# Kernel tuning notes

Measured on AMD Instinct MI355X. Metric: run time of the kernel, lower is better.

Reference implementation:

```python
import jax, jax.numpy as jnp
import numpy as np

EPS = 1e-12  # torch F.normalize eps

def _l2norm(v, axis):
    n = jnp.sqrt(jnp.sum(v * v, axis=axis, keepdims=True))
    return v / jnp.maximum(n, EPS)

def setup_inputs() -> dict:
    key = jax.random.key(0)
    k1, k2, k3, k4, k5 = jax.random.split(key, 5)
    N, C, D, K, R = 8, 1024, 128, 64, 256
    return {
        "x": jax.random.normal(k1, (N, C, D), dtype=jnp.float32),
        "cluster": jax.random.normal(k2, (N, R, D), dtype=jnp.float32),
        "conv_w": jax.random.normal(k3, (K, D), dtype=jnp.float32) * 0.1,
        "conv_b": jax.random.normal(k4, (K,), dtype=jnp.float32) * 0.1,
        "cluster_idx": jax.random.randint(k5, (K,), 0, R),
    }

def reference(x, cluster, conv_w, conv_b, cluster_idx):
    # x: (N, C, D); cluster: (N, R, D); conv_w: (K, D); conv_b: (K,)
    x = _l2norm(x, -1)  # normalize_input, descriptor-wise L2 over dim
    # Conv1d(dim->K, kernel=1) on x^T == matmul over D; softmax over clusters K
    logits = jnp.einsum('ncd,kd->nkc', x, conv_w) + conv_b[None, :, None]
    soft = jax.nn.softmax(logits, axis=1)  # (N, K, C)
    cent = cluster[:, cluster_idx, :]      # (N, K, D) sampled centroids
    # broadcast residual, scaled by soft assignment (no sum over C in V2)
    residual = (x[:, None, :, :] - cent[:, :, None, :]) * soft[..., None]  # (N,K,C,D)
    vlad = jnp.swapaxes(residual, 1, 2)    # (N, C, K, D)
    vlad = _l2norm(vlad, -1)               # intra-normalize over D
    N, C, K, D = vlad.shape
    vlad = vlad.reshape(N, C, K * D)
    return _l2norm(vlad, -1)               # final L2 over flattened K*D
```

## Files before the change

### kernel.cpp

```cpp
#include <hip/hip_runtime.h>

#define N_ 8
#define C_ 1024
#define D_ 128
#define K_ 64
#define R_ 256

typedef float fvec4 __attribute__((ext_vector_type(4)));

__global__ __launch_bounds__(256) void vlad_stream_kernel(
    const float* __restrict__ x,
    const float* __restrict__ cluster,
    const int*   __restrict__ cluster_idx,
    float*       __restrict__ out)
{
    const int n   = blockIdx.x & 7;
    const int c   = blockIdx.x >> 3;
    const int blk = (n << 10) + c;
    const int t   = threadIdx.x;
    const int l   = t & 31;
    const int h   = t >> 5;

    const float* xrow = x + (size_t)blk * D_;
    fvec4 xv = *(const fvec4*)(xrow + l * 4);

    const float* cbase = cluster + (size_t)n * (R_ * D_);
    fvec4 cv[8];
    #pragma unroll
    for (int p = 0; p < 8; ++p) {
        const int k = p * 8 + h;
        cv[p] = *(const fvec4*)(cbase + (size_t)cluster_idx[k] * D_ + l * 4);
    }

    float nx = fmaf(xv.x, xv.x, fmaf(xv.y, xv.y, fmaf(xv.z, xv.z, xv.w * xv.w)));
    #pragma unroll
    for (int m = 1; m <= 16; m <<= 1) nx += __shfl_xor(nx, m, 32);
    const float rinv = 1.0f / fmaxf(sqrtf(nx), 1e-12f);
    xv *= rinv;

    float* orow = out + (size_t)blk * (K_ * D_) + (size_t)t * 4;
    #pragma unroll
    for (int p = 0; p < 8; ++p) {
        fvec4 d = xv - cv[p];
        float ds = fmaf(d.x, d.x, fmaf(d.y, d.y, fmaf(d.z, d.z, d.w * d.w)));
        #pragma unroll
        for (int m = 1; m <= 16; m <<= 1) ds += __shfl_xor(ds, m, 32);
        const float id = 0.125f / fmaxf(sqrtf(ds), 1e-12f);
        *(fvec4*)(orow + (size_t)p * 1024) = d * id;
    }
}

extern "C" void kernel_launch(void* const* d_in, const int* in_sizes, int n_in,
                              void* d_out, int out_size, void* d_ws, size_t ws_size,
                              hipStream_t stream) {
    const float* x           = (const float*)d_in[0];
    const float* cluster     = (const float*)d_in[1];
    const int*   cluster_idx = (const int*)d_in[4];
    float* out = (float*)d_out;

    dim3 grid(N_ * C_), block(256);
    vlad_stream_kernel<<<grid, block, 0, stream>>>(x, cluster, cluster_idx, out);
}
```

Measured before the change: 58.34 us.

## Tile 16 descriptor rows per block and precompute residual norms in shared memory

Each block now handles 16 rows of one batch instead of one row. It normalises the rows into shared memory and computes all 64 residual norms per row in a separate phase with a cooperative reduction. It then streams the scaled residual outputs while reusing the gathered centroid vectors across the 16 rows. The aim is to cut the block count and the redundant centroid gathers, at the cost of extra syncthreads and a serial norm phase in front of the output-write-bound store loop.

Result: no change. 59.30 us (+1.7%).

```diff
diff --git a/kernel.cpp b/kernel.cpp
--- a/kernel.cpp
+++ b/kernel.cpp
@@ -5,48 +5,88 @@
 #define D_ 128
 #define K_ 64
 #define R_ 256
+#define TC 16
+#define XPAD 132
 
 typedef float fvec4 __attribute__((ext_vector_type(4)));
 
-__global__ __launch_bounds__(256) void vlad_stream_kernel(
+__global__ __launch_bounds__(256) void vlad_tiled_kernel(
     const float* __restrict__ x,
     const float* __restrict__ cluster,
     const int*   __restrict__ cluster_idx,
     float*       __restrict__ out)
 {
-    const int n   = blockIdx.x & 7;
-    const int c   = blockIdx.x >> 3;
-    const int blk = (n << 10) + c;
+    __shared__ float xh[TC][XPAD];
+    __shared__ float id_s[TC][K_];
+    __shared__ float part1[TC][16];
+    __shared__ float rinv_s[TC];
+    __shared__ int   coff[K_];
+
+    const int bid = blockIdx.x;
+    const int n   = bid & 7;
+    const int c0  = (bid >> 3) * TC;
     const int t   = threadIdx.x;
-    const int l   = t & 31;
-    const int h   = t >> 5;
 
-    const float* xrow = x + (size_t)blk * D_;
-    fvec4 xv = *(const fvec4*)(xrow + l * 4);
+    if (t < K_) coff[t] = cluster_idx[t] * D_;
 
-    const float* cbase = cluster + (size_t)n * (R_ * D_);
+    const int r = t >> 4, s = t & 15;
+    const float* xrow = x + (size_t)(n * C_ + c0 + r) * D_ + s * 8;
+    fvec4 xa = *(const fvec4*)xrow;
+    fvec4 xb = *(const fvec4*)(xrow + 4);
+    part1[r][s] = xa.x*xa.x + xa.y*xa.y + xa.z*xa.z + xa.w*xa.w
+                + xb.x*xb.x + xb.y*xb.y + xb.z*xb.z + xb.w*xb.w;
+    __syncthreads();
+    if (t < TC) {
+        const fvec4* pp = (const fvec4*)part1[t];
+        fvec4 v = pp[0] + pp[1] + pp[2] + pp[3];
+        rinv_s[t] = 1.0f / fmaxf(sqrtf(v.x + v.y + v.z + v.w), 1e-12f);
+    }
+    __syncthreads();
+    const float rv = rinv_s[r];
+    xa *= rv; xb *= rv;
+    *(fvec4*)&xh[r][s * 8]     = xa;
+    *(fvec4*)&xh[r][s * 8 + 4] = xb;
+    __syncthreads();
+
+    {
+        const int c  = t & 15;
+        const int g  = (t >> 4) & 3;
+        const int kb = t >> 6;
+        const float* cb = cluster + (size_t)n * (R_ * D_) + g * 32;
+        fvec4 xr[8];
+        #pragma unroll
+        for (int j = 0; j < 8; ++j) xr[j] = *(const fvec4*)&xh[c][g * 32 + j * 4];
+        for (int ki = 0; ki < 16; ++ki) {
+            const int k = kb * 16 + ki;
+            const float* crow = cb + coff[k];
+            float acc = 0.f;
+            #pragma unroll
+            for (int j = 0; j < 8; ++j) {
+                fvec4 cv = *(const fvec4*)(crow + j * 4);
+                fvec4 d  = xr[j] - cv;
+                acc = fmaf(d.x, d.x, fmaf(d.y, d.y, fmaf(d.z, d.z, fmaf(d.w, d.w, acc))));
+            }
+            acc += __shfl_xor(acc, 16);
+            acc += __shfl_xor(acc, 32);
+            if (g == 0) id_s[c][k] = 0.125f / fmaxf(sqrtf(acc), 1e-12f);
+        }
+    }
+    __syncthreads();
+
+    const int d4 = t & 31, h = t >> 5;
+    const float* cb2 = cluster + (size_t)n * (R_ * D_) + d4 * 4;
     fvec4 cv[8];
     #pragma unroll
-    for (int p = 0; p < 8; ++p) {
-        const int k = p * 8 + h;
-        cv[p] = *(const fvec4*)(cbase + (size_t)cluster_idx[k] * D_ + l * 4);
-    }
-
-    float nx = fmaf(xv.x, xv.x, fmaf(xv.y, xv.y, fmaf(xv.z, xv.z, xv.w * xv.w)));
-    #pragma unroll
-    for (int m = 1; m <= 16; m <<= 1) nx += __shfl_xor(nx, m, 32);
-    const float rinv = 1.0f / fmaxf(sqrtf(nx), 1e-12f);
-    xv *= rinv;
-
-    float* orow = out + (size_t)blk * (K_ * D_) + (size_t)t * 4;
-    #pragma unroll
-    for (int p = 0; p < 8; ++p) {
-        fvec4 d = xv - cv[p];
-        float ds = fmaf(d.x, d.x, fmaf(d.y, d.y, fmaf(d.z, d.z, d.w * d.w)));
+    for (int q = 0; q < 8; ++q) cv[q] = *(const fvec4*)(cb2 + coff[q * 8 + h]);
+    float* ob = out + (size_t)(n * C_ + c0) * (K_ * D_) + h * D_ + d4 * 4;
+    for (int cc = 0; cc < TC; ++cc) {
+        const fvec4 xv = *(const fvec4*)&xh[cc][d4 * 4];
+        float* oc = ob + (size_t)cc * (K_ * D_);
         #pragma unroll
-        for (int m = 1; m <= 16; m <<= 1) ds += __shfl_xor(ds, m, 32);
-        const float id = 0.125f / fmaxf(sqrtf(ds), 1e-12f);
-        *(fvec4*)(orow + (size_t)p * 1024) = d * id;
+        for (int q = 0; q < 8; ++q) {
+            const float idv = id_s[cc][q * 8 + h];
+            *(fvec4*)(oc + q * 8 * D_) = (xv - cv[q]) * idv;
+        }
     }
 }
 
@@ -58,6 +98,6 @@
     const int*   cluster_idx = (const int*)d_in[4];
     float* out = (float*)d_out;
 
-    dim3 grid(N_ * C_), block(256);
-    vlad_stream_kernel<<<grid, block, 0, stream>>>(x, cluster, cluster_idx, out);
+    dim3 grid(N_ * C_ / TC), block(256);
+    vlad_tiled_kernel<<<grid, block, 0, stream>>>(x, cluster, cluster_idx, out);
 }
```

## Remap threads so each handles a quarter of one cluster row

Applied to the files above, without the earlier changes.

Each thread now owns 32 contiguous floats of one (k) output row. Four threads share a row, so the norm reductions need only two shuffles, and each thread issues a burst of eight consecutive vector stores. This replaces the per-wave 32-lane row layout with its five-step shuffle reductions. The trade-off is that each store instruction's lanes are now strided by 128 bytes, which may reduce write coalescing on a store-bound kernel.

Result: slower. 124.3 us (+113.0%).

```diff
diff --git a/kernel.cpp b/kernel.cpp
--- a/kernel.cpp
+++ b/kernel.cpp
@@ -8,46 +8,58 @@
 
 typedef float fvec4 __attribute__((ext_vector_type(4)));
 
-__global__ __launch_bounds__(256) void vlad_stream_kernel(
+__global__ __launch_bounds__(256) void vlad_burst_kernel(
     const float* __restrict__ x,
     const float* __restrict__ cluster,
     const int*   __restrict__ cluster_idx,
     float*       __restrict__ out)
 {
-    const int n   = blockIdx.x & 7;
-    const int c   = blockIdx.x >> 3;
-    const int blk = (n << 10) + c;
+    const int bid = blockIdx.x;
+    const int n   = bid & 7;
+    const int c   = bid >> 3;
+    const int nc  = (n << 10) + c;
     const int t   = threadIdx.x;
-    const int l   = t & 31;
-    const int h   = t >> 5;
+    const int q   = t & 3;
+    const int k   = t >> 2;
 
-    const float* xrow = x + (size_t)blk * D_;
-    fvec4 xv = *(const fvec4*)(xrow + l * 4);
+    const float* xs = x + (size_t)nc * D_ + q * 32;
+    const int   cid = cluster_idx[k];
+    const float* cs = cluster + ((size_t)n * R_ + cid) * D_ + q * 32;
 
-    const float* cbase = cluster + (size_t)n * (R_ * D_);
-    fvec4 cv[8];
+    fvec4 xr[8], ov[8];
     #pragma unroll
-    for (int p = 0; p < 8; ++p) {
-        const int k = p * 8 + h;
-        cv[p] = *(const fvec4*)(cbase + (size_t)cluster_idx[k] * D_ + l * 4);
+    for (int j = 0; j < 8; ++j) xr[j] = *(const fvec4*)(xs + 4 * j);
+    #pragma unroll
+    for (int j = 0; j < 8; ++j) ov[j] = *(const fvec4*)(cs + 4 * j);
+
+    float nx = 0.f;
+    #pragma unroll
+    for (int j = 0; j < 8; ++j)
+        nx = fmaf(xr[j].x, xr[j].x, fmaf(xr[j].y, xr[j].y,
+             fmaf(xr[j].z, xr[j].z, fmaf(xr[j].w, xr[j].w, nx))));
+    nx += __shfl_xor(nx, 1);
+    nx += __shfl_xor(nx, 2);
+    const float rinv = 1.0f / fmaxf(sqrtf(nx), 1e-12f);
+    #pragma unroll
+    for (int j = 0; j < 8; ++j) xr[j] *= rinv;
+
+    float ds = 0.f;
+    #pragma unroll
+    for (int j = 0; j < 8; ++j) {
+        ov[j] = xr[j] - ov[j];
+        ds = fmaf(ov[j].x, ov[j].x, fmaf(ov[j].y, ov[j].y,
+             fmaf(ov[j].z, ov[j].z, fmaf(ov[j].w, ov[j].w, ds))));
     }
+    ds += __shfl_xor(ds, 1);
+    ds += __shfl_xor(ds, 2);
+    const float idv = 0.125f / fmaxf(sqrtf(ds), 1e-12f);
+    #pragma unroll
+    for (int j = 0; j < 8; ++j) ov[j] *= idv;
 
-    float nx = fmaf(xv.x, xv.x, fmaf(xv.y, xv.y, fmaf(xv.z, xv.z, xv.w * xv.w)));
+    float* ob = out + (size_t)nc * (K_ * D_) + t * 32;
     #pragma unroll
-    for (int m = 1; m <= 16; m <<= 1) nx += __shfl_xor(nx, m, 32);
-    const float rinv = 1.0f / fmaxf(sqrtf(nx), 1e-12f);
-    xv *= rinv;
-
-    float* orow = out + (size_t)blk * (K_ * D_) + (size_t)t * 4;
-    #pragma unroll
-    for (int p = 0; p < 8; ++p) {
-        fvec4 d = xv - cv[p];
-        float ds = fmaf(d.x, d.x, fmaf(d.y, d.y, fmaf(d.z, d.z, d.w * d.w)));
-        #pragma unroll
-        for (int m = 1; m <= 16; m <<= 1) ds += __shfl_xor(ds, m, 32);
-        const float id = 0.125f / fmaxf(sqrtf(ds), 1e-12f);
-        *(fvec4*)(orow + (size_t)p * 1024) = d * id;
-    }
+    for (int j = 0; j < 8; ++j)
+        *(fvec4*)(ob + 4 * j) = ov[j];
 }
 
 extern "C" void kernel_launch(void* const* d_in, const int* in_sizes, int n_in,
@@ -59,5 +71,5 @@
     float* out = (float*)d_out;
 
     dim3 grid(N_ * C_), block(256);
-    vlad_stream_kernel<<<grid, block, 0, stream>>>(x, cluster, cluster_idx, out);
+    vlad_burst_kernel<<<grid, block, 0, stream>>>(x, cluster, cluster_idx, out);
 }
```
